# Performance work log

Measured on AMD Instinct MI355X. Metric: run time of the kernel, lower is better.

## Reference

```python
import jax, jax.numpy as jnp
import numpy as np

N_NODES = 100000
N_EDGES = 1600000
D_IN = 64
D_HID = 64
NEG_SLOPE = 0.01  # torch.nn.LeakyReLU default


def gcn_conv(x, W, b, src, dst, n_nodes):
    h = x @ W  # [N, F_out]
    deg = jnp.zeros((n_nodes,), x.dtype).at[dst].add(jnp.ones((src.shape[0],), x.dtype)) + 1.0
    dinv_sqrt = jax.lax.rsqrt(deg)
    norm = dinv_sqrt[src] * dinv_sqrt[dst]  # [E]
    agg = jnp.zeros_like(h).at[dst].add(norm[:, None] * h[src])
    agg = agg + h * (1.0 / deg)[:, None]  # self-loop contribution: deg^-1/2_i * deg^-1/2_i
    return agg + b


def leaky_relu(v):
    return jnp.where(v >= 0, v, NEG_SLOPE * v)


def setup_inputs() -> dict:
    key = jax.random.key(0)
    ks = jax.random.split(key, 8)
    x = jax.random.normal(ks[0], (N_NODES, D_IN), dtype=jnp.float32)
    edge_index = jax.random.randint(ks[1], (2, N_EDGES), 0, N_NODES, dtype=jnp.int32)
    s = 0.05
    W1 = jax.random.normal(ks[2], (D_IN, D_HID), dtype=jnp.float32) * s
    b1 = jnp.zeros((D_HID,), jnp.float32)
    W2 = jax.random.normal(ks[3], (D_HID, D_HID), dtype=jnp.float32) * s
    b2 = jnp.zeros((D_HID,), jnp.float32)
    W3 = jax.random.normal(ks[4], (D_HID, D_HID), dtype=jnp.float32) * s
    b3 = jnp.zeros((D_HID,), jnp.float32)
    return {"x": x, "W1": W1, "b1": b1, "W2": W2, "b2": b2, "W3": W3, "b3": b3,
            "edge_index": edge_index}


def reference(x, W1, b1, W2, b2, W3, b3, edge_index):
    src, dst = edge_index[0], edge_index[1]
    n = x.shape[0]
    # layer 1: conv -> LeakyReLU -> dropout (identity in eval / reference)
    h = leaky_relu(gcn_conv(x, W1, b1, src, dst, n))
    # layer 2: checkpoint(conv2, ...) -> plain conv, no activation
    h = gcn_conv(h, W2, b2, src, dst, n)
    # layer 3: conv -> LeakyReLU
    h = leaky_relu(gcn_conv(h, W3, b3, src, dst, n))
    return h
```

## Files before the change

kernel.cpp:

```cpp
#include <hip/hip_runtime.h>
#include <hip/hip_fp16.h>
#include <math.h>


constexpr int SHIFT = 8;
constexpr int CHUNK = 4096;
constexpr int BCAP  = 5120;

typedef _Float16 half8 __attribute__((ext_vector_type(8)));
typedef float floatx4 __attribute__((ext_vector_type(4)));

__device__ inline int scan256(int v, int tid, int* wsum, int* total) {
    int lane = tid & 63, w = tid >> 6;
    int inc = v;
#pragma unroll
    for (int off = 1; off < 64; off <<= 1) {
        int t = __shfl_up(inc, off);
        if (lane >= off) inc += t;
    }
    if (lane == 63) wsum[w] = inc;
    __syncthreads();
    int s0 = wsum[0], s1 = wsum[1], s2 = wsum[2], s3 = wsum[3];
    __syncthreads();
    int base = (w > 0 ? s0 : 0) + (w > 1 ? s1 : 0) + (w > 2 ? s2 : 0);
    *total = s0 + s1 + s2 + s3;
    return base + (inc - v);
}

__global__ void k_hist(const int* __restrict__ dst, int E, int NB,
                       int* __restrict__ Bh, int* __restrict__ Bc) {
    __shared__ int h[512];
    int tid = threadIdx.x;
    for (int i = tid; i < 512; i += 256) h[i] = 0;
    __syncthreads();
    int s = blockIdx.x * CHUNK;
    int e = min(s + CHUNK, E);
    for (int i = s + tid; i < e; i += 256) atomicAdd(&h[dst[i] >> SHIFT], 1);
    __syncthreads();
    for (int i = tid; i < NB; i += 256) {
        int v = h[i];
        Bh[(size_t)blockIdx.x * NB + i] = v;
        Bc[(size_t)blockIdx.x * NB + i] = v;
    }
}

__global__ void k_bucket_scan(int* __restrict__ Bh, int B1, int NB,
                              int* __restrict__ total) {
    __shared__ int wsum[4];
    int b = blockIdx.x;
    int tid = threadIdx.x;
    int carry = 0;
    for (int j0 = 0; j0 < B1; j0 += 256) {
        int j = j0 + tid;
        int v = (j < B1) ? Bh[(size_t)j * NB + b] : 0;
        int tot;
        int ex = scan256(v, tid, wsum, &tot);
        if (j < B1) Bh[(size_t)j * NB + b] = ex + carry;
        carry += tot;
    }
    if (tid == 0) total[b] = carry;
}

__global__ void k_base_scan(const int* __restrict__ total, int NB, int E,
                            int* __restrict__ base) {
    __shared__ int wsum[4];
    int tid = threadIdx.x;
    int b0 = 2 * tid, b1 = 2 * tid + 1;
    int v0 = (b0 < NB) ? total[b0] : 0;
    int v1 = (b1 < NB) ? total[b1] : 0;
    int tot;
    int ex = scan256(v0 + v1, tid, wsum, &tot);
    if (b0 < NB) base[b0] = ex;
    if (b1 < NB) base[b1] = ex + v0;
    if (tid == 0) base[NB] = E;
}

__global__ void k_scatter(const int* __restrict__ src, const int* __restrict__ dst,
                          int E, int NB, const int* __restrict__ Bh,
                          const int* __restrict__ Bc, const int* __restrict__ base,
                          unsigned* __restrict__ ebuf) {
    __shared__ int cur[512];
    __shared__ int gb[512];
    __shared__ int wsum[4];
    __shared__ unsigned srec[CHUNK];
    __shared__ int spos[CHUNK];
    int tid = threadIdx.x;
    int j = blockIdx.x;

    int b0 = 2 * tid, b1 = 2 * tid + 1;
    int c0 = (b0 < NB) ? Bc[(size_t)j * NB + b0] : 0;
    int c1 = (b1 < NB) ? Bc[(size_t)j * NB + b1] : 0;
    int tot;
    int ex = scan256(c0 + c1, tid, wsum, &tot);
    if (b0 < NB) {
        cur[b0] = ex;
        gb[b0]  = base[b0] + Bh[(size_t)j * NB + b0] - ex;
    }
    if (b1 < NB) {
        int ex1 = ex + c0;
        cur[b1] = ex1;
        gb[b1]  = base[b1] + Bh[(size_t)j * NB + b1] - ex1;
    }
    __syncthreads();

    int s = j * CHUNK;
    int e = min(s + CHUNK, E);
    for (int i = s + tid; i < e; i += 256) {
        int d = dst[i];
        int b = d >> SHIFT;
        unsigned rec = ((unsigned)(d & 255) << 24) | (unsigned)src[i];
        int lpos = atomicAdd(&cur[b], 1);
        srec[lpos] = rec;
        spos[lpos] = gb[b] + lpos;
    }
    __syncthreads();
    int cntE = e - s;
    for (int t = tid; t < cntE; t += 256) ebuf[spos[t]] = srec[t];
}

__global__ void k_bucket_sort(const unsigned* __restrict__ ebuf,
                              const int* __restrict__ base, int n, int E,
                              int* __restrict__ row_ptr, int* __restrict__ col) {
    __shared__ int cnt[256];
    __shared__ int cur[256];
    __shared__ int wsum[4];
    __shared__ unsigned raw[BCAP];
    __shared__ int sorted[BCAP];
    int b = blockIdx.x;
    int tid = threadIdx.x;
    int s = base[b];
    int e = base[b + 1];
    int len = e - s;
    cnt[tid] = 0;
    __syncthreads();
    if (len <= BCAP) {
        for (int t = tid; t < len; t += 256) {
            unsigned v = ebuf[s + t];
            raw[t] = v;
            atomicAdd(&cnt[v >> 24], 1);
        }
        __syncthreads();
        int tot;
        int ex = scan256(cnt[tid], tid, wsum, &tot);
        int node = (b << SHIFT) | tid;
        if (node < n) row_ptr[node] = s + ex;
        cur[tid] = ex;
        __syncthreads();
        for (int t = tid; t < len; t += 256) {
            unsigned v = raw[t];
            int lpos = atomicAdd(&cur[v >> 24], 1);
            sorted[lpos] = (int)((v & 0x00FFFFFFu) << 7);
        }
        __syncthreads();
        for (int t = tid; t < len; t += 256) col[s + t] = sorted[t];
    } else {
        for (int i = s + tid; i < e; i += 256) atomicAdd(&cnt[ebuf[i] >> 24], 1);
        __syncthreads();
        int tot;
        int ex = scan256(cnt[tid], tid, wsum, &tot);
        int node = (b << SHIFT) | tid;
        if (node < n) row_ptr[node] = s + ex;
        cur[tid] = ex;
        __syncthreads();
        for (int i = s + tid; i < e; i += 256) {
            unsigned v = ebuf[i];
            int lpos = atomicAdd(&cur[v >> 24], 1);
            col[s + lpos] = (int)((v & 0x00FFFFFFu) << 7);
        }
    }
    if (b == 0 && tid == 0) row_ptr[n] = E;
}

__device__ inline void mfma_rows_store(const _Float16* rowS, const _Float16* WtS,
                                       const float* dinvS, int n, int blockRow0,
                                       int tid, __half* __restrict__ HSn) {
    int w = tid >> 6;
    int lane = tid & 63;
    int ar = lane & 15;
    int ks = lane >> 4;

    half8 a1 = *(const half8*)&rowS[ar * 72 + ks * 8];
    half8 a2 = *(const half8*)&rowS[ar * 72 + 32 + ks * 8];
    half8 b1 = *(const half8*)&WtS[(w * 16 + ar) * 72 + ks * 8];
    half8 b2 = *(const half8*)&WtS[(w * 16 + ar) * 72 + 32 + ks * 8];

    floatx4 acc = {0.f, 0.f, 0.f, 0.f};
    acc = __builtin_amdgcn_mfma_f32_16x16x32_f16(a1, b1, acc, 0, 0, 0);
    acc = __builtin_amdgcn_mfma_f32_16x16x32_f16(a2, b2, acc, 0, 0, 0);

    int node0 = (lane >> 4) * 4;
    float4 dv4 = *(const float4*)&dinvS[node0];
    int colg = w * 16 + (lane & 15);
    int base_node = blockRow0 + node0;
#pragma unroll
    for (int reg = 0; reg < 4; reg++) {
        int node_g = base_node + reg;
        if (node_g < n) {
            float dv = (reg == 0) ? dv4.x : (reg == 1) ? dv4.y : (reg == 2) ? dv4.z : dv4.w;
            HSn[(size_t)node_g * 64 + colg] = __float2half(acc[reg] * dv);
        }
    }
}

__device__ inline void stage_wt(const float* __restrict__ Wn, _Float16* WtS, int tid) {
    const float4* W4 = (const float4*)Wn;
#pragma unroll
    for (int j = 0; j < 4; j++) {
        int idx = tid + 256 * j;
        int row = idx >> 4;
        int col0 = (idx & 15) * 4;
        float4 wv = W4[idx];
        WtS[(col0 + 0) * 72 + row] = (_Float16)wv.x;
        WtS[(col0 + 1) * 72 + row] = (_Float16)wv.y;
        WtS[(col0 + 2) * 72 + row] = (_Float16)wv.z;
        WtS[(col0 + 3) * 72 + row] = (_Float16)wv.w;
    }
}

__global__ void k_gemm_scale(const float* __restrict__ X, const float* __restrict__ W,
                             const int* __restrict__ row_ptr, int n,
                             __half* __restrict__ HS) {
    __shared__ _Float16 WtS[64 * 72];
    __shared__ _Float16 rowS[16 * 72];
    __shared__ float dinvS[16];
    int tid = threadIdx.x;
    stage_wt(W, WtS, tid);

    int g = tid >> 4;
    int c = tid & 15;
    int gid = blockIdx.x * 16 + g;
    if (gid < n) {
        float4 xv = *(const float4*)&X[(size_t)gid * 64 + c * 4];
        __half2 h0 = __floats2half2_rn(xv.x, xv.y);
        __half2 h1 = __floats2half2_rn(xv.z, xv.w);
        uint2 pack;
        pack.x = *(const unsigned int*)&h0;
        pack.y = *(const unsigned int*)&h1;
        *(uint2*)&rowS[g * 72 + c * 4] = pack;
        if (c == 0)
            dinvS[g] = rsqrtf(1.0f + (float)(row_ptr[gid + 1] - row_ptr[gid]));
    }
    __syncthreads();
    mfma_rows_store(rowS, WtS, dinvS, n, blockIdx.x * 16, tid, HS);
}

__device__ inline float4 cvt_h4(uint2 v) {
    float2 f0 = __half22float2(*(__half2*)&v.x);
    float2 f1 = __half22float2(*(__half2*)&v.y);
    return make_float4(f0.x, f0.y, f1.x, f1.y);
}

__device__ inline uint2 ld_row(const char* HSb, int boff, int c) {
    return *(const uint2*)(HSb + boff + (c << 3));
}

__device__ inline float4 agg_row(const char* __restrict__ HSb,
                                 const int* __restrict__ col,
                                 int gid, int c, int r0, int r1) {
    float4 a0 = cvt_h4(*(const uint2*)(HSb + ((size_t)gid << 7) + (c << 3)));
    float4 a1 = make_float4(0.f, 0.f, 0.f, 0.f);
    float4 a2 = a1, a3 = a1;
    int e = r0;
    for (; e + 8 <= r1; e += 8) {
        int s0 = col[e + 0], s1 = col[e + 1], s2 = col[e + 2], s3 = col[e + 3];
        int s4 = col[e + 4], s5 = col[e + 5], s6 = col[e + 6], s7 = col[e + 7];
        uint2 v0 = ld_row(HSb, s0, c), v1 = ld_row(HSb, s1, c);
        uint2 v2 = ld_row(HSb, s2, c), v3 = ld_row(HSb, s3, c);
        uint2 v4 = ld_row(HSb, s4, c), v5 = ld_row(HSb, s5, c);
        uint2 v6 = ld_row(HSb, s6, c), v7 = ld_row(HSb, s7, c);
        float4 f0 = cvt_h4(v0), f1 = cvt_h4(v1), f2 = cvt_h4(v2), f3 = cvt_h4(v3);
        float4 f4 = cvt_h4(v4), f5 = cvt_h4(v5), f6 = cvt_h4(v6), f7 = cvt_h4(v7);
        a0.x += f0.x; a0.y += f0.y; a0.z += f0.z; a0.w += f0.w;
        a1.x += f1.x; a1.y += f1.y; a1.z += f1.z; a1.w += f1.w;
        a2.x += f2.x; a2.y += f2.y; a2.z += f2.z; a2.w += f2.w;
        a3.x += f3.x; a3.y += f3.y; a3.z += f3.z; a3.w += f3.w;
        a0.x += f4.x; a0.y += f4.y; a0.z += f4.z; a0.w += f4.w;
        a1.x += f5.x; a1.y += f5.y; a1.z += f5.z; a1.w += f5.w;
        a2.x += f6.x; a2.y += f6.y; a2.z += f6.z; a2.w += f6.w;
        a3.x += f7.x; a3.y += f7.y; a3.z += f7.z; a3.w += f7.w;
    }
    if (e + 4 <= r1) {
        int s0 = col[e + 0], s1 = col[e + 1], s2 = col[e + 2], s3 = col[e + 3];
        uint2 v0 = ld_row(HSb, s0, c), v1 = ld_row(HSb, s1, c);
        uint2 v2 = ld_row(HSb, s2, c), v3 = ld_row(HSb, s3, c);
        float4 f0 = cvt_h4(v0), f1 = cvt_h4(v1), f2 = cvt_h4(v2), f3 = cvt_h4(v3);
        a0.x += f0.x; a0.y += f0.y; a0.z += f0.z; a0.w += f0.w;
        a1.x += f1.x; a1.y += f1.y; a1.z += f1.z; a1.w += f1.w;
        a2.x += f2.x; a2.y += f2.y; a2.z += f2.z; a2.w += f2.w;
        a3.x += f3.x; a3.y += f3.y; a3.z += f3.z; a3.w += f3.w;
        e += 4;
    }
    if (e + 0 < r1) {
        float4 f = cvt_h4(ld_row(HSb, col[e + 0], c));
        a0.x += f.x; a0.y += f.y; a0.z += f.z; a0.w += f.w;
    }
    if (e + 1 < r1) {
        float4 f = cvt_h4(ld_row(HSb, col[e + 1], c));
        a1.x += f.x; a1.y += f.y; a1.z += f.z; a1.w += f.w;
    }
    if (e + 2 < r1) {
        float4 f = cvt_h4(ld_row(HSb, col[e + 2], c));
        a2.x += f.x; a2.y += f.y; a2.z += f.z; a2.w += f.w;
    }
    float4 s;
    s.x = (a0.x + a1.x) + (a2.x + a3.x);
    s.y = (a0.y + a1.y) + (a2.y + a3.y);
    s.z = (a0.z + a1.z) + (a2.z + a3.z);
    s.w = (a0.w + a1.w) + (a2.w + a3.w);
    return s;
}

template <bool RELU>
__global__ void k_agg_gemm(const __half* __restrict__ HS, const int* __restrict__ row_ptr,
                           const int* __restrict__ col, const float* __restrict__ bias,
                           const float* __restrict__ Wn, int n,
                           __half* __restrict__ HSn) {
    __shared__ _Float16 WtS[64 * 72];
    __shared__ _Float16 rowS[16 * 72];
    __shared__ float dinvS[16];
    int tid = threadIdx.x;
    stage_wt(Wn, WtS, tid);

    int g = tid >> 4;
    int c = tid & 15;
    int gid = blockIdx.x * 16 + g;

    if (gid < n) {
        const char* __restrict__ HSb = (const char*)HS;
        int r0 = row_ptr[gid];
        int r1 = row_ptr[gid + 1];
        float4 s = agg_row(HSb, col, gid, c, r0, r1);
        float deg = 1.0f + (float)(r1 - r0);
        float dinv = rsqrtf(deg);
        float4 bv = *(const float4*)&bias[4 * c];
        float vx = dinv * s.x + bv.x;
        float vy = dinv * s.y + bv.y;
        float vz = dinv * s.z + bv.z;
        float vw = dinv * s.w + bv.w;
        if (RELU) {
            vx = (vx >= 0.f) ? vx : 0.01f * vx;
            vy = (vy >= 0.f) ? vy : 0.01f * vy;
            vz = (vz >= 0.f) ? vz : 0.01f * vz;
            vw = (vw >= 0.f) ? vw : 0.01f * vw;
        }
        __half2 h0 = __floats2half2_rn(vx, vy);
        __half2 h1 = __floats2half2_rn(vz, vw);
        uint2 pack;
        pack.x = *(const unsigned int*)&h0;
        pack.y = *(const unsigned int*)&h1;
        *(uint2*)&rowS[g * 72 + c * 4] = pack;
        if (c == 0) dinvS[g] = dinv;
    }
    __syncthreads();
    mfma_rows_store(rowS, WtS, dinvS, n, blockIdx.x * 16, tid, HSn);
}

__global__ void k_agg_out(const __half* __restrict__ HS, const int* __restrict__ row_ptr,
                          const int* __restrict__ col, const float* __restrict__ bias,
                          int n, float* __restrict__ out) {
    int gid = (int)((blockIdx.x * (unsigned)blockDim.x + threadIdx.x) >> 4);
    if (gid >= n) return;
    int c = threadIdx.x & 15;
    const char* __restrict__ HSb = (const char*)HS;
    int r0 = row_ptr[gid];
    int r1 = row_ptr[gid + 1];
    float4 s = agg_row(HSb, col, gid, c, r0, r1);
    float deg = 1.0f + (float)(r1 - r0);
    float dinv = rsqrtf(deg);
    float4 bv = *(const float4*)&bias[4 * c];
    float vx = dinv * s.x + bv.x;
    float vy = dinv * s.y + bv.y;
    float vz = dinv * s.z + bv.z;
    float vw = dinv * s.w + bv.w;
    vx = (vx >= 0.f) ? vx : 0.01f * vx;
    vy = (vy >= 0.f) ? vy : 0.01f * vy;
    vz = (vz >= 0.f) ? vz : 0.01f * vz;
    vw = (vw >= 0.f) ? vw : 0.01f * vw;
    *(float4*)&out[(size_t)gid * 64 + 4 * c] = make_float4(vx, vy, vz, vw);
}

static inline size_t align256(size_t x) { return (x + 255) & ~(size_t)255; }

extern "C" void kernel_launch(void* const* d_in, const int* in_sizes, int n_in,
                              void* d_out, int out_size, void* d_ws, size_t ws_size,
                              hipStream_t stream) {
    const float* x  = (const float*)d_in[0];
    const float* W1 = (const float*)d_in[1];
    const float* b1 = (const float*)d_in[2];
    const float* W2 = (const float*)d_in[3];
    const float* b2 = (const float*)d_in[4];
    const float* W3 = (const float*)d_in[5];
    const float* b3 = (const float*)d_in[6];
    const int* edge = (const int*)d_in[7];

    int n = in_sizes[0] / 64;
    int E = in_sizes[7] / 2;
    const int* srcp = edge;
    const int* dstp = edge + E;

    int NB = (n + 255) >> SHIFT;
    int B1 = (E + CHUNK - 1) / CHUNK;

    char* ws = (char*)d_ws;
    int* row_ptr   = (int*)ws;      ws += align256((size_t)(n + 1) * 4);
    int* Bh        = (int*)ws;      ws += align256((size_t)B1 * NB * 4);
    int* Bc        = (int*)ws;      ws += align256((size_t)B1 * NB * 4);
    int* total     = (int*)ws;      ws += align256((size_t)NB * 4);
    int* base      = (int*)ws;      ws += align256((size_t)(NB + 1) * 4);
    unsigned* ebuf = (unsigned*)ws; ws += align256((size_t)E * 4);
    int* col       = (int*)ws;      ws += align256((size_t)E * 4);
    __half* hs_a   = (__half*)ws;   ws += align256((size_t)n * 64 * 2);
    __half* hs_b   = (__half*)ws;   ws += align256((size_t)n * 64 * 2);
    float* out     = (float*)d_out;

    k_hist<<<B1, 256, 0, stream>>>(dstp, E, NB, Bh, Bc);
    k_bucket_scan<<<NB, 256, 0, stream>>>(Bh, B1, NB, total);
    k_base_scan<<<1, 256, 0, stream>>>(total, NB, E, base);
    k_scatter<<<B1, 256, 0, stream>>>(srcp, dstp, E, NB, Bh, Bc, base, ebuf);
    k_bucket_sort<<<NB, 256, 0, stream>>>(ebuf, base, n, E, row_ptr, col);

    int blocks16 = (n + 15) / 16;

    k_gemm_scale<<<blocks16, 256, 0, stream>>>(x, W1, row_ptr, n, hs_a);
    k_agg_gemm<true><<<blocks16, 256, 0, stream>>>(hs_a, row_ptr, col, b1, W2, n, hs_b);
    k_agg_gemm<false><<<blocks16, 256, 0, stream>>>(hs_b, row_ptr, col, b2, W3, n, hs_a);
    k_agg_out<<<blocks16, 256, 0, stream>>>(hs_a, row_ptr, col, b3, n, out);
}
```

Baseline: 160.4 us.

## Fuse CSR build kernels into one cooperative kernel; load W fragments into registers

The five CSR-construction kernels (histogram, per-bucket scan, base scan, scatter, bucket sort) are merged into a single cooperative kernel separated by grid-wide syncs, and the base-offset scan is recomputed redundantly per block instead of in its own launch. The goal is to remove launch overhead and inter-kernel gaps. Separately, the GEMM kernels no longer stage the transposed W into LDS; each lane loads its MFMA B fragments straight from global memory into registers. The risks are grid.sync cost, the need for every block of a grid of max(B1,NB)≈391 blocks to be co-resident with the larger shared-memory union, and strided scalar global loads of W in every block.

After: 316.3 us. +97.2%, slower.

```diff
diff --git a/kernel.cpp b/kernel.cpp
--- a/kernel.cpp
+++ b/kernel.cpp
@@ -1,6 +1,9 @@
 #include <hip/hip_runtime.h>
 #include <hip/hip_fp16.h>
+#include <hip/hip_cooperative_groups.h>
 #include <math.h>
+
+namespace cg = cooperative_groups;
 
 
 constexpr int SHIFT = 8;
@@ -27,152 +30,153 @@
     return base + (inc - v);
 }
 
-__global__ void k_hist(const int* __restrict__ dst, int E, int NB,
-                       int* __restrict__ Bh, int* __restrict__ Bc) {
+__global__ void k_build(const int* __restrict__ src, const int* __restrict__ dst,
+                        int E, int n, int NB, int B1,
+                        int* __restrict__ Bh, int* __restrict__ Bc,
+                        int* __restrict__ total, unsigned* __restrict__ ebuf,
+                        int* __restrict__ col, int* __restrict__ row_ptr) {
+    cg::grid_group grid = cg::this_grid();
+    __shared__ union {
+        struct { unsigned srec[CHUNK]; int spos[CHUNK]; } sc;
+        struct { unsigned raw[BCAP]; int sorted[BCAP]; } so;
+    } U;
     __shared__ int h[512];
-    int tid = threadIdx.x;
-    for (int i = tid; i < 512; i += 256) h[i] = 0;
-    __syncthreads();
-    int s = blockIdx.x * CHUNK;
-    int e = min(s + CHUNK, E);
-    for (int i = s + tid; i < e; i += 256) atomicAdd(&h[dst[i] >> SHIFT], 1);
-    __syncthreads();
-    for (int i = tid; i < NB; i += 256) {
-        int v = h[i];
-        Bh[(size_t)blockIdx.x * NB + i] = v;
-        Bc[(size_t)blockIdx.x * NB + i] = v;
-    }
-}
-
-__global__ void k_bucket_scan(int* __restrict__ Bh, int B1, int NB,
-                              int* __restrict__ total) {
-    __shared__ int wsum[4];
-    int b = blockIdx.x;
-    int tid = threadIdx.x;
-    int carry = 0;
-    for (int j0 = 0; j0 < B1; j0 += 256) {
-        int j = j0 + tid;
-        int v = (j < B1) ? Bh[(size_t)j * NB + b] : 0;
-        int tot;
-        int ex = scan256(v, tid, wsum, &tot);
-        if (j < B1) Bh[(size_t)j * NB + b] = ex + carry;
-        carry += tot;
-    }
-    if (tid == 0) total[b] = carry;
-}
-
-__global__ void k_base_scan(const int* __restrict__ total, int NB, int E,
-                            int* __restrict__ base) {
-    __shared__ int wsum[4];
-    int tid = threadIdx.x;
-    int b0 = 2 * tid, b1 = 2 * tid + 1;
-    int v0 = (b0 < NB) ? total[b0] : 0;
-    int v1 = (b1 < NB) ? total[b1] : 0;
-    int tot;
-    int ex = scan256(v0 + v1, tid, wsum, &tot);
-    if (b0 < NB) base[b0] = ex;
-    if (b1 < NB) base[b1] = ex + v0;
-    if (tid == 0) base[NB] = E;
-}
-
-__global__ void k_scatter(const int* __restrict__ src, const int* __restrict__ dst,
-                          int E, int NB, const int* __restrict__ Bh,
-                          const int* __restrict__ Bc, const int* __restrict__ base,
-                          unsigned* __restrict__ ebuf) {
     __shared__ int cur[512];
     __shared__ int gb[512];
     __shared__ int wsum[4];
-    __shared__ unsigned srec[CHUNK];
-    __shared__ int spos[CHUNK];
     int tid = threadIdx.x;
-    int j = blockIdx.x;
-
-    int b0 = 2 * tid, b1 = 2 * tid + 1;
-    int c0 = (b0 < NB) ? Bc[(size_t)j * NB + b0] : 0;
-    int c1 = (b1 < NB) ? Bc[(size_t)j * NB + b1] : 0;
-    int tot;
-    int ex = scan256(c0 + c1, tid, wsum, &tot);
-    if (b0 < NB) {
-        cur[b0] = ex;
-        gb[b0]  = base[b0] + Bh[(size_t)j * NB + b0] - ex;
-    }
-    if (b1 < NB) {
-        int ex1 = ex + c0;
-        cur[b1] = ex1;
-        gb[b1]  = base[b1] + Bh[(size_t)j * NB + b1] - ex1;
-    }
-    __syncthreads();
-
-    int s = j * CHUNK;
-    int e = min(s + CHUNK, E);
-    for (int i = s + tid; i < e; i += 256) {
-        int d = dst[i];
-        int b = d >> SHIFT;
-        unsigned rec = ((unsigned)(d & 255) << 24) | (unsigned)src[i];
-        int lpos = atomicAdd(&cur[b], 1);
-        srec[lpos] = rec;
-        spos[lpos] = gb[b] + lpos;
-    }
-    __syncthreads();
-    int cntE = e - s;
-    for (int t = tid; t < cntE; t += 256) ebuf[spos[t]] = srec[t];
-}
-
-__global__ void k_bucket_sort(const unsigned* __restrict__ ebuf,
-                              const int* __restrict__ base, int n, int E,
-                              int* __restrict__ row_ptr, int* __restrict__ col) {
-    __shared__ int cnt[256];
-    __shared__ int cur[256];
-    __shared__ int wsum[4];
-    __shared__ unsigned raw[BCAP];
-    __shared__ int sorted[BCAP];
-    int b = blockIdx.x;
-    int tid = threadIdx.x;
-    int s = base[b];
-    int e = base[b + 1];
-    int len = e - s;
-    cnt[tid] = 0;
-    __syncthreads();
-    if (len <= BCAP) {
-        for (int t = tid; t < len; t += 256) {
-            unsigned v = ebuf[s + t];
-            raw[t] = v;
-            atomicAdd(&cnt[v >> 24], 1);
-        }
+    int blk = blockIdx.x;
+
+    if (blk < B1) {
+        for (int i = tid; i < 512; i += 256) h[i] = 0;
         __syncthreads();
+        int s = blk * CHUNK, e = min(s + CHUNK, E);
+        for (int i = s + tid; i < e; i += 256) atomicAdd(&h[dst[i] >> SHIFT], 1);
+        __syncthreads();
+        for (int i = tid; i < NB; i += 256) {
+            int v = h[i];
+            Bh[(size_t)blk * NB + i] = v;
+            Bc[(size_t)blk * NB + i] = v;
+        }
+    }
+    grid.sync();
+
+    if (blk < NB) {
+        int carry = 0;
+        for (int j0 = 0; j0 < B1; j0 += 256) {
+            int j = j0 + tid;
+            int v = (j < B1) ? Bh[(size_t)j * NB + blk] : 0;
+            int tot;
+            int ex = scan256(v, tid, wsum, &tot);
+            if (j < B1) Bh[(size_t)j * NB + blk] = ex + carry;
+            carry += tot;
+        }
+        if (tid == 0) total[blk] = carry;
+    }
+    grid.sync();
+
+    if (blk < B1) {
+        int b0 = 2 * tid, b1i = 2 * tid + 1;
+        int t0 = (b0 < NB) ? total[b0] : 0;
+        int t1 = (b1i < NB) ? total[b1i] : 0;
         int tot;
-        int ex = scan256(cnt[tid], tid, wsum, &tot);
-        int node = (b << SHIFT) | tid;
-        if (node < n) row_ptr[node] = s + ex;
-        cur[tid] = ex;
+        int exb = scan256(t0 + t1, tid, wsum, &tot);
+        int base0 = exb, base1 = exb + t0;
+        int c0 = (b0 < NB) ? Bc[(size_t)blk * NB + b0] : 0;
+        int c1 = (b1i < NB) ? Bc[(size_t)blk * NB + b1i] : 0;
+        int exl = scan256(c0 + c1, tid, wsum, &tot);
+        if (b0 < NB) {
+            cur[b0] = exl;
+            gb[b0]  = base0 + Bh[(size_t)blk * NB + b0] - exl;
+        }
+        if (b1i < NB) {
+            int l1 = exl + c0;
+            cur[b1i] = l1;
+            gb[b1i]  = base1 + Bh[(size_t)blk * NB + b1i] - l1;
+        }
         __syncthreads();
-        for (int t = tid; t < len; t += 256) {
-            unsigned v = raw[t];
-            int lpos = atomicAdd(&cur[v >> 24], 1);
-            sorted[lpos] = (int)((v & 0x00FFFFFFu) << 7);
+        int s = blk * CHUNK, e = min(s + CHUNK, E);
+        for (int i = s + tid; i < e; i += 256) {
+            int d = dst[i];
+            int b = d >> SHIFT;
+            unsigned rec = ((unsigned)(d & 255) << 24) | (unsigned)src[i];
+            int lpos = atomicAdd(&cur[b], 1);
+            U.sc.srec[lpos] = rec;
+            U.sc.spos[lpos] = gb[b] + lpos;
         }
         __syncthreads();
-        for (int t = tid; t < len; t += 256) col[s + t] = sorted[t];
-    } else {
-        for (int i = s + tid; i < e; i += 256) atomicAdd(&cnt[ebuf[i] >> 24], 1);
+        int cntE = e - s;
+        for (int t = tid; t < cntE; t += 256) ebuf[U.sc.spos[t]] = U.sc.srec[t];
+    }
+    grid.sync();
+
+    if (blk < NB) {
+        int b0 = 2 * tid, b1i = 2 * tid + 1;
+        int t0 = (b0 < NB) ? total[b0] : 0;
+        int t1 = (b1i < NB) ? total[b1i] : 0;
+        int tot;
+        int exb = scan256(t0 + t1, tid, wsum, &tot);
+        if (b0 < NB) gb[b0] = exb;
+        if (b1i < NB) gb[b1i] = exb + t0;
+        h[tid] = 0;
         __syncthreads();
-        int tot;
-        int ex = scan256(cnt[tid], tid, wsum, &tot);
-        int node = (b << SHIFT) | tid;
-        if (node < n) row_ptr[node] = s + ex;
-        cur[tid] = ex;
-        __syncthreads();
-        for (int i = s + tid; i < e; i += 256) {
-            unsigned v = ebuf[i];
-            int lpos = atomicAdd(&cur[v >> 24], 1);
-            col[s + lpos] = (int)((v & 0x00FFFFFFu) << 7);
-        }
-    }
-    if (b == 0 && tid == 0) row_ptr[n] = E;
-}
-
-__device__ inline void mfma_rows_store(const _Float16* rowS, const _Float16* WtS,
-                                       const float* dinvS, int n, int blockRow0,
+        int s = gb[blk];
+        int len = total[blk];
+        int e = s + len;
+        if (len <= BCAP) {
+            for (int t = tid; t < len; t += 256) {
+                unsigned v = ebuf[s + t];
+                U.so.raw[t] = v;
+                atomicAdd(&h[v >> 24], 1);
+            }
+            __syncthreads();
+            int ex = scan256(h[tid], tid, wsum, &tot);
+            int node = (blk << SHIFT) | tid;
+            if (node < n) row_ptr[node] = s + ex;
+            cur[tid] = ex;
+            __syncthreads();
+            for (int t = tid; t < len; t += 256) {
+                unsigned v = U.so.raw[t];
+                int lpos = atomicAdd(&cur[v >> 24], 1);
+                U.so.sorted[lpos] = (int)((v & 0x00FFFFFFu) << 7);
+            }
+            __syncthreads();
+            for (int t = tid; t < len; t += 256) col[s + t] = U.so.sorted[t];
+        } else {
+            for (int i = s + tid; i < e; i += 256) atomicAdd(&h[ebuf[i] >> 24], 1);
+            __syncthreads();
+            int ex = scan256(h[tid], tid, wsum, &tot);
+            int node = (blk << SHIFT) | tid;
+            if (node < n) row_ptr[node] = s + ex;
+            cur[tid] = ex;
+            __syncthreads();
+            for (int i = s + tid; i < e; i += 256) {
+                unsigned v = ebuf[i];
+                int lpos = atomicAdd(&cur[v >> 24], 1);
+                col[s + lpos] = (int)((v & 0x00FFFFFFu) << 7);
+            }
+        }
+        if (blk == 0 && tid == 0) row_ptr[n] = E;
+    }
+}
+
+__device__ inline void load_bfrag(const float* __restrict__ W, int tid,
+                                  half8* b1, half8* b2) {
+    int lane = tid & 63;
+    int colg = (tid >> 6) * 16 + (lane & 15);
+    int k0 = (lane >> 4) * 8;
+    half8 x1, x2;
+#pragma unroll
+    for (int j = 0; j < 8; j++) {
+        x1[j] = (_Float16)W[(k0 + j) * 64 + colg];
+        x2[j] = (_Float16)W[(k0 + 32 + j) * 64 + colg];
+    }
+    *b1 = x1;
+    *b2 = x2;
+}
+
+__device__ inline void mfma_rows_store(const _Float16* rowS, const float* dinvS,
+                                       half8 b1, half8 b2, int n, int blockRow0,
                                        int tid, __half* __restrict__ HSn) {
     int w = tid >> 6;
     int lane = tid & 63;
@@ -181,8 +185,6 @@
 
     half8 a1 = *(const half8*)&rowS[ar * 72 + ks * 8];
     half8 a2 = *(const half8*)&rowS[ar * 72 + 32 + ks * 8];
-    half8 b1 = *(const half8*)&WtS[(w * 16 + ar) * 72 + ks * 8];
-    half8 b2 = *(const half8*)&WtS[(w * 16 + ar) * 72 + 32 + ks * 8];
 
     floatx4 acc = {0.f, 0.f, 0.f, 0.f};
     acc = __builtin_amdgcn_mfma_f32_16x16x32_f16(a1, b1, acc, 0, 0, 0);
@@ -202,29 +204,15 @@
     }
 }
 
-__device__ inline void stage_wt(const float* __restrict__ Wn, _Float16* WtS, int tid) {
-    const float4* W4 = (const float4*)Wn;
-#pragma unroll
-    for (int j = 0; j < 4; j++) {
-        int idx = tid + 256 * j;
-        int row = idx >> 4;
-        int col0 = (idx & 15) * 4;
-        float4 wv = W4[idx];
-        WtS[(col0 + 0) * 72 + row] = (_Float16)wv.x;
-        WtS[(col0 + 1) * 72 + row] = (_Float16)wv.y;
-        WtS[(col0 + 2) * 72 + row] = (_Float16)wv.z;
-        WtS[(col0 + 3) * 72 + row] = (_Float16)wv.w;
-    }
-}
-
 __global__ void k_gemm_scale(const float* __restrict__ X, const float* __restrict__ W,
                              const int* __restrict__ row_ptr, int n,
                              __half* __restrict__ HS) {
-    __shared__ _Float16 WtS[64 * 72];
     __shared__ _Float16 rowS[16 * 72];
     __shared__ float dinvS[16];
     int tid = threadIdx.x;
-    stage_wt(W, WtS, tid);
+
+    half8 b1, b2;
+    load_bfrag(W, tid, &b1, &b2);
 
     int g = tid >> 4;
     int c = tid & 15;
@@ -241,7 +229,7 @@
             dinvS[g] = rsqrtf(1.0f + (float)(row_ptr[gid + 1] - row_ptr[gid]));
     }
     __syncthreads();
-    mfma_rows_store(rowS, WtS, dinvS, n, blockIdx.x * 16, tid, HS);
+    mfma_rows_store(rowS, dinvS, b1, b2, n, blockIdx.x * 16, tid, HS);
 }
 
 __device__ inline float4 cvt_h4(uint2 v) {
@@ -315,11 +303,12 @@
                            const int* __restrict__ col, const float* __restrict__ bias,
                            const float* __restrict__ Wn, int n,
                            __half* __restrict__ HSn) {
-    __shared__ _Float16 WtS[64 * 72];
     __shared__ _Float16 rowS[16 * 72];
     __shared__ float dinvS[16];
     int tid = threadIdx.x;
-    stage_wt(Wn, WtS, tid);
+
+    half8 b1, b2;
+    load_bfrag(Wn, tid, &b1, &b2);
 
     int g = tid >> 4;
     int c = tid & 15;
@@ -352,7 +341,7 @@
         if (c == 0) dinvS[g] = dinv;
     }
     __syncthreads();
-    mfma_rows_store(rowS, WtS, dinvS, n, blockIdx.x * 16, tid, HSn);
+    mfma_rows_store(rowS, dinvS, b1, b2, n, blockIdx.x * 16, tid, HSn);
 }
 
 __global__ void k_agg_out(const __half* __restrict__ HS, const int* __restrict__ row_ptr,
@@ -406,18 +395,24 @@
     int* Bh        = (int*)ws;      ws += align256((size_t)B1 * NB * 4);
     int* Bc        = (int*)ws;      ws += align256((size_t)B1 * NB * 4);
     int* total     = (int*)ws;      ws += align256((size_t)NB * 4);
-    int* base      = (int*)ws;      ws += align256((size_t)(NB + 1) * 4);
     unsigned* ebuf = (unsigned*)ws; ws += align256((size_t)E * 4);
     int* col       = (int*)ws;      ws += align256((size_t)E * 4);
     __half* hs_a   = (__half*)ws;   ws += align256((size_t)n * 64 * 2);
     __half* hs_b   = (__half*)ws;   ws += align256((size_t)n * 64 * 2);
     float* out     = (float*)d_out;
 
-    k_hist<<<B1, 256, 0, stream>>>(dstp, E, NB, Bh, Bc);
-    k_bucket_scan<<<NB, 256, 0, stream>>>(Bh, B1, NB, total);
-    k_base_scan<<<1, 256, 0, stream>>>(total, NB, E, base);
-    k_scatter<<<B1, 256, 0, stream>>>(srcp, dstp, E, NB, Bh, Bc, base, ebuf);
-    k_bucket_sort<<<NB, 256, 0, stream>>>(ebuf, base, n, E, row_ptr, col);
+    {
+        int G = (B1 > NB) ? B1 : NB;
+        int En = E, nn = n, NBn = NB, B1n = B1;
+        const int* srcp_l = srcp;
+        const int* dstp_l = dstp;
+        int* Bh_l = Bh; int* Bc_l = Bc; int* total_l = total;
+        unsigned* ebuf_l = ebuf; int* col_l = col; int* rp_l = row_ptr;
+        void* args[] = {(void*)&srcp_l, (void*)&dstp_l, (void*)&En, (void*)&nn,
+                        (void*)&NBn, (void*)&B1n, (void*)&Bh_l, (void*)&Bc_l,
+                        (void*)&total_l, (void*)&ebuf_l, (void*)&col_l, (void*)&rp_l};
+        hipLaunchCooperativeKernel((void*)k_build, dim3(G), dim3(256), args, 0, stream);
+    }
 
     int blocks16 = (n + 15) / 16;
 
```
